# Kernel tuning notes

Measured on AMD Instinct MI355X. Metric: run time of the kernel, lower is better.

The kernel has to match this reference:

```python
import jax, jax.numpy as jnp
import numpy as np

B, S, D, H = 2, 2048, 1024, 16
DH = D // H  # dim_per_head = 64


def setup_inputs() -> dict:
    key = jax.random.key(0)
    ks = jax.random.split(key, 12)
    std = 1.0 / np.sqrt(D)
    inp = {
        "key": jax.random.normal(ks[0], (B, S, D), jnp.float32),
        "value": jax.random.normal(ks[1], (B, S, D), jnp.float32),
        "query": jax.random.normal(ks[2], (B, S, D), jnp.float32),
        "mask": jax.random.randint(ks[3], (B, S, S), 0, 2) == 1,
        "Wk": jax.random.normal(ks[4], (D, D), jnp.float32) * std,
        "bk": jnp.zeros((D,), jnp.float32),
        "Wv": jax.random.normal(ks[5], (D, D), jnp.float32) * std,
        "bv": jnp.zeros((D,), jnp.float32),
        "Wq": jax.random.normal(ks[6], (D, D), jnp.float32) * std,
        "bq": jnp.zeros((D,), jnp.float32),
        "Wo": jax.random.normal(ks[7], (D, D), jnp.float32) * std,
        "bo": jnp.zeros((D,), jnp.float32),
    }
    return inp


def _shape(x):
    # (B, L, D) -> (B, H, L, DH)
    return x.reshape(B, -1, H, DH).transpose(0, 2, 1, 3)


def reference(key, value, query, mask, Wk, bk, Wv, bv, Wq, bq, Wo, bo):
    k = _shape(key @ Wk.T + bk)      # (B,H,S,DH)
    v = _shape(value @ Wv.T + bv)    # (B,H,S,DH)
    q = _shape(query @ Wq.T + bq)    # (B,H,S,DH)
    q = q / jnp.sqrt(jnp.asarray(DH, q.dtype))
    scores = jnp.einsum("bhqd,bhkd->bhqk", q, k).astype(jnp.float32)
    scores = jnp.where(mask[:, None, :, :], jnp.float32(-1e18), scores)
    attn = jax.nn.softmax(scores, axis=-1).astype(q.dtype)  # (B,H,S,S)
    # dropout p=0.0 -> identity
    ctx = jnp.einsum("bhqk,bhkd->bhqd", attn, v)
    ctx = ctx.transpose(0, 2, 1, 3).reshape(B, -1, D)
    output = ctx @ Wo.T + bo
    top_attn = attn[:, 0, :, :]
    return output, top_attn
```

## Files before the change

kernel.cpp:

```cpp
#include <hip/hip_runtime.h>

constexpr int BB = 2, SS = 2048, DD = 1024, HH = 16, DHH = 64;

typedef __attribute__((ext_vector_type(4))) float f32x4;
typedef __attribute__((ext_vector_type(8))) __bf16 bf16x8;
typedef __attribute__((ext_vector_type(8))) unsigned short us8;

__device__ __forceinline__ unsigned short f32_to_bf16(float f) {
    unsigned int u = __float_as_uint(f);
    u += 0x7fffu + ((u >> 16) & 1u);
    return (unsigned short)(u >> 16);
}

__device__ __forceinline__ ushort2 pk_bf16(float a, float b) {
#if __has_builtin(__builtin_amdgcn_cvt_pk_bf16_f32)
    typedef __attribute__((ext_vector_type(2))) __bf16 bf16x2;
    bf16x2 r = __builtin_amdgcn_cvt_pk_bf16_f32(a, b);
    return *(ushort2*)&r;
#else
    ushort2 r; r.x = f32_to_bf16(a); r.y = f32_to_bf16(b); return r;
#endif
}
__device__ __forceinline__ ushort4 pk_bf16x4(float a, float b, float c, float d) {
    const ushort2 lo = pk_bf16(a, b), hi = pk_bf16(c, d);
    ushort4 r; r.x = lo.x; r.y = lo.y; r.z = hi.x; r.w = hi.y;
    return r;
}

__device__ __forceinline__ f32x4 mfma_bf16(bf16x8 a, bf16x8 b, f32x4 c) {
    return __builtin_amdgcn_mfma_f32_16x16x32_bf16(a, b, c, 0, 0, 0);
}

__device__ __forceinline__ void stage16(const void* g, void* l) {
    typedef const __attribute__((address_space(1))) unsigned int gas_t;
    typedef __attribute__((address_space(3))) unsigned int las_t;
    __builtin_amdgcn_global_load_lds((gas_t*)(unsigned long long)g,
                                     (las_t*)(unsigned int)(unsigned long long)l,
                                     16, 0, 0);
}

__global__ __launch_bounds__(256) void cvt_bf16(const float* __restrict__ src,
                                                unsigned short* __restrict__ dst) {
    const size_t i = ((size_t)blockIdx.x * 256 + threadIdx.x) * 8;
    const float4 a = *(const float4*)(src + i);
    const float4 b = *(const float4*)(src + i + 4);
    ushort4 lo = pk_bf16x4(a.x, a.y, a.z, a.w);
    ushort4 hi = pk_bf16x4(b.x, b.y, b.z, b.w);
    us8 o;
    o[0] = lo.x; o[1] = lo.y; o[2] = lo.z; o[3] = lo.w;
    o[4] = hi.x; o[5] = hi.y; o[6] = hi.z; o[7] = hi.w;
    *(us8*)(dst + i) = o;
}

__global__ __launch_bounds__(256) void mask_pack(const int* __restrict__ mask,
                                                 unsigned long long* __restrict__ pm) {
    const int t = threadIdx.x;
    const size_t chunk = (size_t)blockIdx.x * 4 + (t >> 6);
    const int lane = t & 63;
    const int v = mask[chunk * 64 + lane];
    const unsigned long long b = __ballot(v != 0);
    if (lane == 0) pm[chunk] = b;
}

template <int MODE>
__global__ __launch_bounds__(256) void gemm_nt(const unsigned short* __restrict__ A,
                                               const unsigned short* __restrict__ Wb,
                                               const float* __restrict__ bias,
                                               void* __restrict__ outp,
                                               float scale) {
    constexpr int K = DD;
    __shared__ __align__(16) unsigned short Ash[2][128][64];
    __shared__ __align__(16) unsigned short Bsh[2][64][64];

    const int id = blockIdx.x;
    const int nid = (id & 7) * 64 + (id >> 3);
    const int n0 = (nid & 15) * 64;
    const int m0 = (nid >> 4) * 128;

    const int t = threadIdx.x;
    const int lane = t & 63, w = t >> 6;
    const int l15 = lane & 15, quad = lane >> 4;
    const int wm = (w >> 1) * 64, wn = (w & 1) * 32;

    const int srow = lane >> 3;
    const int scol8 = ((lane & 7) ^ srow) * 8;
    const unsigned short* Ag = A + (size_t)(m0 + w * 32 + srow) * K + scol8;
    const unsigned short* Bg = Wb + (size_t)(n0 + w * 16 + srow) * K + scol8;

    f32x4 acc[4][2] = {};

#pragma unroll
    for (int j = 0; j < 4; ++j) stage16(Ag + (size_t)j * 8 * K, &Ash[0][w * 32 + j * 8][0]);
#pragma unroll
    for (int j = 0; j < 2; ++j) stage16(Bg + (size_t)j * 8 * K, &Bsh[0][w * 16 + j * 8][0]);

    for (int kk = 0; kk < K / 64; ++kk) {
        const int cur = kk & 1;
        if (kk < K / 64 - 1) {
            const size_t ko = (size_t)(kk + 1) * 64;
#pragma unroll
            for (int j = 0; j < 4; ++j)
                stage16(Ag + (size_t)j * 8 * K + ko, &Ash[cur ^ 1][w * 32 + j * 8][0]);
#pragma unroll
            for (int j = 0; j < 2; ++j)
                stage16(Bg + (size_t)j * 8 * K + ko, &Bsh[cur ^ 1][w * 16 + j * 8][0]);
            __asm__ volatile("s_waitcnt vmcnt(6)" ::: "memory");
        } else {
            __asm__ volatile("s_waitcnt vmcnt(0)" ::: "memory");
        }
        __builtin_amdgcn_s_barrier();
        __builtin_amdgcn_sched_barrier(0);

        const unsigned short* Ab = &Ash[cur][0][0];
        const unsigned short* Bb = &Bsh[cur][0][0];

#pragma unroll
        for (int s = 0; s < 2; ++s) {
            const int ch = ((s * 4 + quad) ^ (l15 & 7)) * 8;
            bf16x8 af[4], bfr[2];
#pragma unroll
            for (int mi = 0; mi < 4; ++mi)
                af[mi] = *(const bf16x8*)&Ab[(wm + mi * 16 + l15) * 64 + ch];
#pragma unroll
            for (int ni = 0; ni < 2; ++ni)
                bfr[ni] = *(const bf16x8*)&Bb[(wn + ni * 16 + l15) * 64 + ch];
            __builtin_amdgcn_s_setprio(1);
#pragma unroll
            for (int mi = 0; mi < 4; ++mi)
#pragma unroll
                for (int ni = 0; ni < 2; ++ni)
                    acc[mi][ni] = mfma_bf16(af[mi], bfr[ni], acc[mi][ni]);
            __builtin_amdgcn_s_setprio(0);
        }
        __builtin_amdgcn_sched_barrier(0);
        __builtin_amdgcn_s_barrier();
        __builtin_amdgcn_sched_barrier(0);
    }

#pragma unroll
    for (int ni = 0; ni < 2; ++ni) {
        const int c = n0 + wn + ni * 16 + l15;
        const float bs = bias[c];
#pragma unroll
        for (int mi = 0; mi < 4; ++mi) {
#pragma unroll
            for (int r = 0; r < 4; ++r) {
                const int mrow = m0 + wm + mi * 16 + quad * 4 + r;
                const float val = (acc[mi][ni][r] + bs) * scale;
                if (MODE == 2) {
                    ((float*)outp)[(size_t)mrow * DD + c] = val;
                } else {
                    const int bi2 = mrow >> 11, si = mrow & (SS - 1);
                    const int hi2 = c >> 6, di = c & (DHH - 1);
                    unsigned short* o = (unsigned short*)outp;
                    if (MODE == 0)
                        o[((size_t)(bi2 * HH + hi2) * SS + si) * DHH + di] = f32_to_bf16(val);
                    else
                        o[((size_t)(bi2 * HH + hi2) * DHH + di) * SS + si] = f32_to_bf16(val);
                }
            }
        }
    }
}

__global__ __launch_bounds__(512, 4) void flash_attn(const unsigned short* __restrict__ qws,
                                                     const unsigned short* __restrict__ kws,
                                                     const unsigned short* __restrict__ vws,
                                                     const unsigned long long* __restrict__ pm,
                                                     unsigned short* __restrict__ ctx,
                                                     float2* __restrict__ stats) {
    __shared__ __align__(16) unsigned short Ksh[2][64][64];
    __shared__ __align__(16) unsigned short Vsh[2][64][64];
    __shared__ __align__(16) unsigned short Psh[8][16][72];

    constexpr int NQT = SS / 128;
    const int id = blockIdx.x;
    const int nid = (id & 7) * 64 + (id >> 3);
    const int qt = nid % NQT;
    const int bh = nid / NQT;
    const int bi = bh / HH, hi = bh % HH;

    const int t = threadIdx.x;
    const int lane = t & 63, w = t >> 6;
    const int l15 = lane & 15, quad = lane >> 4;
    const int sh4 = quad * 4;
    const int xk = quad ^ (l15 & 7);

    const unsigned short* qp = qws + (size_t)bh * SS * DHH;
    const unsigned short* kp = kws + (size_t)bh * SS * DHH;
    const unsigned short* vp = vws + (size_t)bh * DHH * SS;

    const int q_loc = qt * 128 + w * 16 + l15;
    const bf16x8 bq0 = *(const bf16x8*)(qp + (size_t)q_loc * DHH + quad * 8);
    const bf16x8 bq1 = *(const bf16x8*)(qp + (size_t)q_loc * DHH + 32 + quad * 8);
    const unsigned long long* pmrow = pm + ((size_t)bi * SS + q_loc) * (SS / 64);

    const int srow = lane >> 3;
    const int scol = (lane & 7) ^ srow;
    const unsigned short* kg = kp + (size_t)(w * 8 + srow) * DHH + scol * 8;
    const unsigned short* vg = vp + (size_t)(w * 8 + srow) * SS + scol * 8;

    f32x4 accO[4] = {};
    float m_run = -1e30f, l_run = 0.f;
    const float NEG_INF = -__builtin_inff();

    unsigned long long mcur = pmrow[0];
    stage16(kg, &Ksh[0][w * 8][0]);
    stage16(vg, &Vsh[0][w * 8][0]);

    constexpr int NT = SS / 64;
    for (int kt = 0; kt < NT; ++kt) {
        const int cur = kt & 1;
        unsigned long long mnxt = 0;
        if (kt < NT - 1) {
            mnxt = pmrow[kt + 1];
            stage16(kg + (size_t)(kt + 1) * 64 * DHH, &Ksh[cur ^ 1][w * 8][0]);
            stage16(vg + (size_t)(kt + 1) * 64,       &Vsh[cur ^ 1][w * 8][0]);
            __asm__ volatile("s_waitcnt vmcnt(3)" ::: "memory");
        } else {
            __asm__ volatile("s_waitcnt vmcnt(0)" ::: "memory");
        }
        __builtin_amdgcn_s_barrier();
        __builtin_amdgcn_sched_barrier(0);

        const unsigned short* Kb = &Ksh[cur][0][0];
        const unsigned short* Vb = &Vsh[cur][0][0];

        bf16x8 ak0[4], ak1[4];
#pragma unroll
        for (int i = 0; i < 4; ++i) {
            ak0[i] = *(const bf16x8*)&Kb[(i * 16 + l15) * 64 + xk * 8];
            ak1[i] = *(const bf16x8*)&Kb[(i * 16 + l15) * 64 + (xk ^ 4) * 8];
        }

        const unsigned int mlo = ((unsigned int)mcur) >> sh4;
        const unsigned int mhi = ((unsigned int)(mcur >> 32)) >> sh4;

        float sc[4][4];
        __builtin_amdgcn_s_setprio(1);
#pragma unroll
        for (int i = 0; i < 4; ++i) {
            f32x4 s4 = {};
            s4 = mfma_bf16(ak0[i], bq0, s4);
            s4 = mfma_bf16(ak1[i], bq1, s4);
            const unsigned int mw = (i & 2) ? mhi : mlo;
#pragma unroll
            for (int r = 0; r < 4; ++r)
                sc[i][r] = ((mw >> ((i & 1) * 16 + r)) & 1u) ? NEG_INF : s4[r];
        }
        __builtin_amdgcn_s_setprio(0);

        bf16x8 av0[4], av1[4];
#pragma unroll
        for (int i = 0; i < 4; ++i) {
            av0[i] = *(const bf16x8*)&Vb[(i * 16 + l15) * 64 + xk * 8];
            av1[i] = *(const bf16x8*)&Vb[(i * 16 + l15) * 64 + (xk ^ 4) * 8];
        }

        float tm = sc[0][0];
#pragma unroll
        for (int i = 0; i < 4; ++i)
#pragma unroll
            for (int r = 0; r < 4; ++r) tm = fmaxf(tm, sc[i][r]);
        tm = fmaxf(tm, __shfl_xor(tm, 16));
        tm = fmaxf(tm, __shfl_xor(tm, 32));

        const bool nodefer = !__all(tm <= m_run + 8.0f);
        const float mn = nodefer ? fmaxf(m_run, tm) : m_run;

        float rs = 0.f;
#pragma unroll
        for (int i = 0; i < 4; ++i)
#pragma unroll
            for (int r = 0; r < 4; ++r) {
                const float p = __builtin_amdgcn_exp2f(sc[i][r] - mn);
                sc[i][r] = p;
                rs += p;
            }
        rs += __shfl_xor(rs, 16);
        rs += __shfl_xor(rs, 32);

        if (nodefer) {
            const float alpha = __builtin_amdgcn_exp2f(m_run - mn);
            l_run = l_run * alpha + rs;
            m_run = mn;
#pragma unroll
            for (int i = 0; i < 4; ++i) accO[i] *= alpha;
        } else {
            l_run += rs;
        }

#pragma unroll
        for (int i = 0; i < 4; ++i)
            *(ushort4*)&Psh[w][l15][i * 16 + sh4] =
                pk_bf16x4(sc[i][0], sc[i][1], sc[i][2], sc[i][3]);
        __asm__ volatile("s_waitcnt lgkmcnt(0)" ::: "memory");

        const bf16x8 p0 = *(const bf16x8*)&Psh[w][l15][quad * 8];
        const bf16x8 p1 = *(const bf16x8*)&Psh[w][l15][32 + quad * 8];
        __builtin_amdgcn_s_setprio(1);
#pragma unroll
        for (int i = 0; i < 4; ++i) {
            accO[i] = mfma_bf16(av0[i], p0, accO[i]);
            accO[i] = mfma_bf16(av1[i], p1, accO[i]);
        }
        __builtin_amdgcn_s_setprio(0);

        __builtin_amdgcn_sched_barrier(0);
        __builtin_amdgcn_s_barrier();
        __builtin_amdgcn_sched_barrier(0);
        mcur = mnxt;
    }

    const float inv = 1.0f / l_run;
    unsigned short* cb = ctx + ((size_t)(bi * SS) + q_loc) * DD + hi * DHH;
#pragma unroll
    for (int i = 0; i < 4; ++i)
        *(ushort4*)&cb[i * 16 + sh4] = pk_bf16x4(accO[i][0] * inv, accO[i][1] * inv,
                                                 accO[i][2] * inv, accO[i][3] * inv);

    if (hi == 0 && quad == 0) {
        float2 st; st.x = m_run; st.y = l_run;
        stats[(size_t)bi * SS + q_loc] = st;
    }
}

__global__ __launch_bounds__(256) void prob_h0(const unsigned short* __restrict__ q0,
                                               const unsigned short* __restrict__ k0,
                                               const unsigned long long* __restrict__ pm,
                                               const float2* __restrict__ stats,
                                               float* __restrict__ outp) {
    __shared__ __align__(16) unsigned short Ksh[64][72];

    const int kc = blockIdx.x & 3;
    const int qt = (blockIdx.x >> 2) & 31;
    const int bi = blockIdx.x >> 7;

    const int t = threadIdx.x;
    const int lane = t & 63, w = t >> 6;
    const int l15 = lane & 15, quad = lane >> 4;
    const int sh4 = quad * 4;

    const int q = qt * 64 + w * 16 + l15;
    const unsigned short* qp = q0 + ((size_t)bi * SS + q) * DHH;
    const bf16x8 bq0 = *(const bf16x8*)(qp + quad * 8);
    const bf16x8 bq1 = *(const bf16x8*)(qp + 32 + quad * 8);

    const unsigned short* kp = k0 + (size_t)bi * SS * DHH;
    const unsigned long long* pmq = pm + ((size_t)bi * SS + q) * (SS / 64);
    float* orow = outp + ((size_t)bi * SS + q) * SS;

    const float2 st = stats[(size_t)bi * SS + q];
    const float M = st.x;
    const float invL = 1.0f / st.y;

    for (int kt = 0; kt < 8; ++kt) {
        const int key0 = kc * 512 + kt * 64;
        __syncthreads();
#pragma unroll
        for (int hf = 0; hf < 2; ++hf) {
            const int v = t + hf * 256;
            const int row = v >> 3, off = (v & 7) * 8;
            *(us8*)&Ksh[row][off] = *(const us8*)(kp + (size_t)(key0 + row) * DHH + off);
        }
        __syncthreads();

        const unsigned long long m64 = pmq[kc * 8 + kt];
        const unsigned int mlo = ((unsigned int)m64) >> sh4;
        const unsigned int mhi = ((unsigned int)(m64 >> 32)) >> sh4;

#pragma unroll
        for (int i = 0; i < 4; ++i) {
            const bf16x8 ak0 = *(const bf16x8*)&Ksh[i * 16 + l15][quad * 8];
            const bf16x8 ak1 = *(const bf16x8*)&Ksh[i * 16 + l15][32 + quad * 8];
            f32x4 s4 = {};
            s4 = mfma_bf16(ak0, bq0, s4);
            s4 = mfma_bf16(ak1, bq1, s4);
            const unsigned int mw = (i & 2) ? mhi : mlo;
            float4 ov;
#pragma unroll
            for (int r = 0; r < 4; ++r) {
                const float p = __builtin_amdgcn_exp2f(s4[r] - M) * invL;
                ((float*)&ov)[r] = ((mw >> ((i & 1) * 16 + r)) & 1u) ? 0.0f : p;
            }
            *(float4*)&orow[key0 + i * 16 + sh4] = ov;
        }
    }
}

extern "C" void kernel_launch(void* const* d_in, const int* in_sizes, int n_in,
                              void* d_out, int out_size, void* d_ws, size_t ws_size,
                              hipStream_t stream) {
    const float* key_   = (const float*)d_in[0];
    const float* value_ = (const float*)d_in[1];
    const float* query_ = (const float*)d_in[2];
    const int*   mask_  = (const int*)d_in[3];
    const float* Wk = (const float*)d_in[4];
    const float* bk = (const float*)d_in[5];
    const float* Wv = (const float*)d_in[6];
    const float* bv = (const float*)d_in[7];
    const float* Wq = (const float*)d_in[8];
    const float* bq = (const float*)d_in[9];
    const float* Wo = (const float*)d_in[10];
    const float* bo = (const float*)d_in[11];

    constexpr size_t XS  = (size_t)BB * SS * DD;
    constexpr size_t WSZ = (size_t)DD * DD;

    float* out_f = (float*)d_out;
    unsigned short* scratch = (unsigned short*)(out_f + XS);
    unsigned short* qws = scratch;
    unsigned short* kws = qws + XS;
    unsigned short* vws = kws + XS;
    unsigned short* ctx = vws + XS;

    unsigned short* q0 = (unsigned short*)d_ws;
    unsigned short* k0 = q0 + (size_t)BB * SS * DHH;
    unsigned long long* pm = (unsigned long long*)(k0 + (size_t)BB * SS * DHH);
    float2* stats = (float2*)(pm + (size_t)BB * SS * (SS / 64));

    unsigned short* Xq  = (unsigned short*)out_f;
    unsigned short* Xk  = Xq + XS;
    unsigned short* Xv  = kws;
    unsigned short* Wqb = ctx;
    unsigned short* Wkb = Wqb + WSZ;
    unsigned short* Wvb = Wkb + WSZ;
    unsigned short* Wob = qws;

    mask_pack<<<BB * SS * (SS / 64) / 4, 256, 0, stream>>>(mask_, pm);

    cvt_bf16<<<XS / 2048, 256, 0, stream>>>(query_, Xq);
    cvt_bf16<<<XS / 2048, 256, 0, stream>>>(key_,   Xk);
    cvt_bf16<<<XS / 2048, 256, 0, stream>>>(value_, Xv);
    cvt_bf16<<<WSZ / 2048, 256, 0, stream>>>(Wq, Wqb);
    cvt_bf16<<<WSZ / 2048, 256, 0, stream>>>(Wk, Wkb);
    cvt_bf16<<<WSZ / 2048, 256, 0, stream>>>(Wv, Wvb);

    const float qscale = 0.125f * 1.4426950408889634f;

    gemm_nt<0><<<512, 256, 0, stream>>>(Xq, Wqb, bq, qws, qscale);
    gemm_nt<1><<<512, 256, 0, stream>>>(Xv, Wvb, bv, vws, 1.0f);
    gemm_nt<0><<<512, 256, 0, stream>>>(Xk, Wkb, bk, kws, 1.0f);

    for (int b = 0; b < BB; ++b) {
        hipMemcpyAsync(q0 + (size_t)b * SS * DHH, qws + (size_t)(b * HH) * SS * DHH,
                       (size_t)SS * DHH * sizeof(unsigned short),
                       hipMemcpyDeviceToDevice, stream);
        hipMemcpyAsync(k0 + (size_t)b * SS * DHH, kws + (size_t)(b * HH) * SS * DHH,
                       (size_t)SS * DHH * sizeof(unsigned short),
                       hipMemcpyDeviceToDevice, stream);
    }

    flash_attn<<<BB * HH * (SS / 128), 512, 0, stream>>>(qws, kws, vws, pm, ctx, stats);

    cvt_bf16<<<WSZ / 2048, 256, 0, stream>>>(Wo, Wob);
    gemm_nt<2><<<512, 256, 0, stream>>>(ctx, Wob, bo, out_f, 1.0f);

    prob_h0<<<BB * 32 * 4, 256, 0, stream>>>(q0, k0, pm, stats, out_f + XS);
}
```

Baseline: 318.3 us.

## Fuse prep kernels, merge Q/V GEMMs, write head-0 copies in epilogue

Merges the mask packing and the six bf16 conversions into one prep kernel, and runs the Q and V projections in one launch of 1024 blocks. Head-0 Q and K are now written by the GEMM epilogue, which replaces the separate device-to-device memcpys. prob_h0 now uses 512 blocks with a swizzled index so that each block handles 256 keys instead of 512. The aim is to cut launch overhead and raise GPU occupancy. In exchange the GEMM epilogue does extra conditional stores, and mode is now a runtime value rather than a template parameter.

```diff
diff --git a/kernel.cpp b/kernel.cpp
--- a/kernel.cpp
+++ b/kernel.cpp
@@ -39,9 +39,9 @@
                                      16, 0, 0);
 }
 
-__global__ __launch_bounds__(256) void cvt_bf16(const float* __restrict__ src,
-                                                unsigned short* __restrict__ dst) {
-    const size_t i = ((size_t)blockIdx.x * 256 + threadIdx.x) * 8;
+__device__ __forceinline__ void cvt_block(const float* __restrict__ src,
+                                          unsigned short* __restrict__ dst, int blk) {
+    const size_t i = ((size_t)blk * 256 + threadIdx.x) * 8;
     const float4 a = *(const float4*)(src + i);
     const float4 b = *(const float4*)(src + i + 4);
     ushort4 lo = pk_bf16x4(a.x, a.y, a.z, a.w);
@@ -52,28 +52,59 @@
     *(us8*)(dst + i) = o;
 }
 
-__global__ __launch_bounds__(256) void mask_pack(const int* __restrict__ mask,
-                                                 unsigned long long* __restrict__ pm) {
-    const int t = threadIdx.x;
-    const size_t chunk = (size_t)blockIdx.x * 4 + (t >> 6);
-    const int lane = t & 63;
-    const int v = mask[chunk * 64 + lane];
-    const unsigned long long b = __ballot(v != 0);
-    if (lane == 0) pm[chunk] = b;
-}
-
-template <int MODE>
-__global__ __launch_bounds__(256) void gemm_nt(const unsigned short* __restrict__ A,
-                                               const unsigned short* __restrict__ Wb,
-                                               const float* __restrict__ bias,
-                                               void* __restrict__ outp,
-                                               float scale) {
+__global__ __launch_bounds__(256) void cvt_bf16(const float* __restrict__ src,
+                                                unsigned short* __restrict__ dst) {
+    cvt_block(src, dst, blockIdx.x);
+}
+
+__global__ __launch_bounds__(256) void prep(const float* __restrict__ q,
+                                            const float* __restrict__ k,
+                                            const float* __restrict__ v,
+                                            const float* __restrict__ Wq,
+                                            const float* __restrict__ Wk,
+                                            const float* __restrict__ Wv,
+                                            unsigned short* __restrict__ Xq,
+                                            unsigned short* __restrict__ Xk,
+                                            unsigned short* __restrict__ Xv,
+                                            unsigned short* __restrict__ Wqb,
+                                            unsigned short* __restrict__ Wkb,
+                                            unsigned short* __restrict__ Wvb,
+                                            const int* __restrict__ mask,
+                                            unsigned long long* __restrict__ pm) {
+    const int id = blockIdx.x;
+    if (id < 6144) {
+        const int sel = id >> 11, blk = id & 2047;
+        cvt_block(sel == 0 ? q : (sel == 1 ? k : v),
+                  sel == 0 ? Xq : (sel == 1 ? Xk : Xv), blk);
+    } else if (id < 7680) {
+        const int wid = id - 6144;
+        const int sel = wid >> 9, blk = wid & 511;
+        cvt_block(sel == 0 ? Wq : (sel == 1 ? Wk : Wv),
+                  sel == 0 ? Wqb : (sel == 1 ? Wkb : Wvb), blk);
+    } else {
+        const int mid = id - 7680;
+        const int t = threadIdx.x, lane = t & 63;
+#pragma unroll
+        for (int it = 0; it < 4; ++it) {
+            const size_t chunk = (size_t)mid * 16 + it * 4 + (t >> 6);
+            const int val = mask[chunk * 64 + lane];
+            const unsigned long long b = __ballot(val != 0);
+            if (lane == 0) pm[chunk] = b;
+        }
+    }
+}
+
+__device__ __forceinline__ void gemm_body(int mode,
+                                          const unsigned short* __restrict__ A,
+                                          const unsigned short* __restrict__ Wb,
+                                          const float* __restrict__ bias,
+                                          void* __restrict__ outp,
+                                          float scale, int nid,
+                                          unsigned short* __restrict__ h0) {
     constexpr int K = DD;
     __shared__ __align__(16) unsigned short Ash[2][128][64];
     __shared__ __align__(16) unsigned short Bsh[2][64][64];
 
-    const int id = blockIdx.x;
-    const int nid = (id & 7) * 64 + (id >> 3);
     const int n0 = (nid & 15) * 64;
     const int m0 = (nid >> 4) * 128;
 
@@ -147,20 +178,54 @@
             for (int r = 0; r < 4; ++r) {
                 const int mrow = m0 + wm + mi * 16 + quad * 4 + r;
                 const float val = (acc[mi][ni][r] + bs) * scale;
-                if (MODE == 2) {
+                if (mode == 2) {
                     ((float*)outp)[(size_t)mrow * DD + c] = val;
                 } else {
                     const int bi2 = mrow >> 11, si = mrow & (SS - 1);
                     const int hi2 = c >> 6, di = c & (DHH - 1);
                     unsigned short* o = (unsigned short*)outp;
-                    if (MODE == 0)
-                        o[((size_t)(bi2 * HH + hi2) * SS + si) * DHH + di] = f32_to_bf16(val);
-                    else
-                        o[((size_t)(bi2 * HH + hi2) * DHH + di) * SS + si] = f32_to_bf16(val);
+                    const unsigned short v16 = f32_to_bf16(val);
+                    if (mode == 0) {
+                        o[((size_t)(bi2 * HH + hi2) * SS + si) * DHH + di] = v16;
+                        if (h0 != nullptr && hi2 == 0)
+                            h0[((size_t)bi2 * SS + si) * DHH + di] = v16;
+                    } else {
+                        o[((size_t)(bi2 * HH + hi2) * DHH + di) * SS + si] = v16;
+                    }
                 }
             }
         }
     }
+}
+
+__global__ __launch_bounds__(256) void gemm_qv(const unsigned short* __restrict__ Xq,
+                                               const unsigned short* __restrict__ Wqb,
+                                               const float* __restrict__ bq,
+                                               unsigned short* __restrict__ qws,
+                                               float qscale,
+                                               unsigned short* __restrict__ q0,
+                                               const unsigned short* __restrict__ Xv,
+                                               const unsigned short* __restrict__ Wvb,
+                                               const float* __restrict__ bv,
+                                               unsigned short* __restrict__ vws) {
+    const int id = blockIdx.x;
+    const int gid = id >> 9, id9 = id & 511;
+    const int nid = (id9 & 7) * 64 + (id9 >> 3);
+    gemm_body(gid, gid ? Xv : Xq, gid ? Wvb : Wqb, gid ? bv : bq,
+              gid ? (void*)vws : (void*)qws, gid ? 1.0f : qscale, nid,
+              gid ? nullptr : q0);
+}
+
+template <int MODE>
+__global__ __launch_bounds__(256) void gemm_one(const unsigned short* __restrict__ A,
+                                                const unsigned short* __restrict__ Wb,
+                                                const float* __restrict__ bias,
+                                                void* __restrict__ outp,
+                                                float scale,
+                                                unsigned short* __restrict__ h0) {
+    const int id = blockIdx.x;
+    const int nid = (id & 7) * 64 + (id >> 3);
+    gemm_body(MODE, A, Wb, bias, outp, scale, nid, h0);
 }
 
 __global__ __launch_bounds__(512, 4) void flash_attn(const unsigned short* __restrict__ qws,
@@ -332,9 +397,11 @@
                                                float* __restrict__ outp) {
     __shared__ __align__(16) unsigned short Ksh[64][72];
 
-    const int kc = blockIdx.x & 3;
-    const int qt = (blockIdx.x >> 2) & 31;
-    const int bi = blockIdx.x >> 7;
+    const int id = blockIdx.x;
+    const int nid = (id & 7) * 64 + (id >> 3);
+    const int kc = nid & 7;
+    const int qt = (nid >> 3) & 31;
+    const int bi = nid >> 8;
 
     const int t = threadIdx.x;
     const int lane = t & 63, w = t >> 6;
@@ -354,8 +421,8 @@
     const float M = st.x;
     const float invL = 1.0f / st.y;
 
-    for (int kt = 0; kt < 8; ++kt) {
-        const int key0 = kc * 512 + kt * 64;
+    for (int kt = 0; kt < 4; ++kt) {
+        const int key0 = kc * 256 + kt * 64;
         __syncthreads();
 #pragma unroll
         for (int hf = 0; hf < 2; ++hf) {
@@ -365,7 +432,7 @@
         }
         __syncthreads();
 
-        const unsigned long long m64 = pmq[kc * 8 + kt];
+        const unsigned long long m64 = pmq[kc * 4 + kt];
         const unsigned int mlo = ((unsigned int)m64) >> sh4;
         const unsigned int mhi = ((unsigned int)(m64 >> 32)) >> sh4;
 
@@ -427,34 +494,21 @@
     unsigned short* Wvb = Wkb + WSZ;
     unsigned short* Wob = qws;
 
-    mask_pack<<<BB * SS * (SS / 64) / 4, 256, 0, stream>>>(mask_, pm);
-
-    cvt_bf16<<<XS / 2048, 256, 0, stream>>>(query_, Xq);
-    cvt_bf16<<<XS / 2048, 256, 0, stream>>>(key_,   Xk);
-    cvt_bf16<<<XS / 2048, 256, 0, stream>>>(value_, Xv);
-    cvt_bf16<<<WSZ / 2048, 256, 0, stream>>>(Wq, Wqb);
-    cvt_bf16<<<WSZ / 2048, 256, 0, stream>>>(Wk, Wkb);
-    cvt_bf16<<<WSZ / 2048, 256, 0, stream>>>(Wv, Wvb);
-
     const float qscale = 0.125f * 1.4426950408889634f;
 
-    gemm_nt<0><<<512, 256, 0, stream>>>(Xq, Wqb, bq, qws, qscale);
-    gemm_nt<1><<<512, 256, 0, stream>>>(Xv, Wvb, bv, vws, 1.0f);
-    gemm_nt<0><<<512, 256, 0, stream>>>(Xk, Wkb, bk, kws, 1.0f);
-
-    for (int b = 0; b < BB; ++b) {
-        hipMemcpyAsync(q0 + (size_t)b * SS * DHH, qws + (size_t)(b * HH) * SS * DHH,
-                       (size_t)SS * DHH * sizeof(unsigned short),
-                       hipMemcpyDeviceToDevice, stream);
-        hipMemcpyAsync(k0 + (size_t)b * SS * DHH, kws + (size_t)(b * HH) * SS * DHH,
-                       (size_t)SS * DHH * sizeof(unsigned short),
-                       hipMemcpyDeviceToDevice, stream);
-    }
+    prep<<<15872, 256, 0, stream>>>(query_, key_, value_, Wq, Wk, Wv,
+                                    Xq, Xk, Xv, Wqb, Wkb, Wvb, mask_, pm);
+
+    gemm_qv<<<1024, 256, 0, stream>>>(Xq, Wqb, bq, qws, qscale, q0,
+                                      Xv, Wvb, bv, vws);
+
+    gemm_one<0><<<512, 256, 0, stream>>>(Xk, Wkb, bk, kws, 1.0f, k0);
 
     flash_attn<<<BB * HH * (SS / 128), 512, 0, stream>>>(qws, kws, vws, pm, ctx, stats);
 
     cvt_bf16<<<WSZ / 2048, 256, 0, stream>>>(Wo, Wob);
-    gemm_nt<2><<<512, 256, 0, stream>>>(ctx, Wob, bo, out_f, 1.0f);
-
-    prob_h0<<<BB * 32 * 4, 256, 0, stream>>>(q0, k0, pm, stats, out_f + XS);
-}
+
+    gemm_one<2><<<512, 256, 0, stream>>>(ctx, Wob, bo, out_f, 1.0f, nullptr);
+
+    prob_h0<<<512, 256, 0, stream>>>(q0, k0, pm, stats, out_f + XS);
+}
```

New measurement: 302.9 us. 1.05x faster.
